# Kernel optimization log

Hardware: AMD Instinct MI355X
Metric: run time of the kernel (lower is better)

Reference implementation:

```python
import jax, jax.numpy as jnp
import numpy as np

N = 50000      # nodes
E = 800000     # edges (before self-loops)
DIN = 2        # dim_input
DEMB = 128     # dim_embedding
H = 8          # n_heads
DV = 16        # dim_values (H*DV == DEMB)
DH = 512       # dim_hidden
L = 2          # n_att_layers
K = 10         # APPNP steps
ALPHA = 0.1
EPS = 1e-5     # BatchNorm eps
NEG_SLOPE = 0.2  # GAT leaky_relu slope


def setup_inputs() -> dict:
    key = jax.random.key(0)
    ks = jax.random.split(key, 16)
    s = 0.05
    inp = {}
    inp["x"] = jax.random.normal(ks[0], (N, DIN), jnp.float32)
    inp["J"] = jax.random.uniform(ks[1], (N, 1), jnp.float32)
    inp["edge_index"] = jax.random.randint(ks[2], (2, E), 0, N, jnp.int32)
    # Lin1: Linear(dim_input+1, dim_embedding)
    inp["lin0_w"] = jax.random.normal(ks[3], (DIN + 1, DEMB), jnp.float32) * s
    inp["lin0_b"] = jnp.zeros((DEMB,), jnp.float32)
    # Per attention layer (stacked over L):
    inp["gat_w"]   = jax.random.normal(ks[4], (L, DEMB, H * DV), jnp.float32) * s
    inp["att_src"] = jax.random.normal(ks[5], (L, H, DV), jnp.float32) * s
    inp["att_dst"] = jax.random.normal(ks[6], (L, H, DV), jnp.float32) * s
    inp["lin1_w"]  = jax.random.normal(ks[7], (L, DV, DEMB), jnp.float32) * s
    inp["bn1_g"]   = jnp.ones((L, DEMB), jnp.float32)
    inp["bn1_b"]   = jnp.zeros((L, DEMB), jnp.float32)
    inp["lin2_w"]  = jax.random.normal(ks[8], (L, DEMB, DH), jnp.float32) * s
    inp["lin2_b"]  = jnp.zeros((L, DH), jnp.float32)
    inp["lin3_w"]  = jax.random.normal(ks[9], (L, DH, DEMB), jnp.float32) * s
    inp["lin3_b"]  = jnp.zeros((L, DEMB), jnp.float32)
    inp["bn2_g"]   = jnp.ones((L, DEMB), jnp.float32)
    inp["bn2_b"]   = jnp.zeros((L, DEMB), jnp.float32)
    return inp


def _bn(z, g, b):
    # BatchNorm1d over nodes, training-mode batch statistics (biased var)
    mu = z.mean(0)
    var = jnp.mean((z - mu) ** 2, axis=0)
    return g * (z - mu) * jax.lax.rsqrt(var + EPS) + b


def reference(x, J, edge_index, lin0_w, lin0_b, gat_w, att_src, att_dst,
              lin1_w, bn1_g, bn1_b, lin2_w, lin2_b, lin3_w, lin3_b,
              bn2_g, bn2_b):
    # add self-loops (PyG GATConv and APPNP defaults)
    loop = jnp.arange(N, dtype=edge_index.dtype)
    src = jnp.concatenate([edge_index[0], loop])  # message source j
    dst = jnp.concatenate([edge_index[1], loop])  # message target i

    h = jnp.concatenate([x, J], axis=1) @ lin0_w + lin0_b  # [N, DEMB]

    for l in range(L):
        # ---- GATConv ----
        xl = (h @ gat_w[l]).reshape(N, H, DV)                # [N,H,DV]
        a_s = (xl * att_src[l]).sum(-1)                      # [N,H]
        a_d = (xl * att_dst[l]).sum(-1)                      # [N,H]
        e = jax.nn.leaky_relu(a_s[src] + a_d[dst], NEG_SLOPE)  # [E',H]
        e = e - jax.ops.segment_max(e, dst, num_segments=N)[dst]
        ee = jnp.exp(e)
        alpha = ee / jax.ops.segment_sum(ee, dst, num_segments=N)[dst]
        msg = xl[src] * alpha[:, :, None]                    # [E',H,DV]
        gat_out = jax.ops.segment_sum(msg, dst, num_segments=N)  # [N,H,DV]
        # lin1 per head then sum over heads
        hsum = jnp.einsum('nhc,cd->nd', gat_out, lin1_w[l])  # [N,DEMB]
        h1 = _bn(h + hsum, bn1_g[l], bn1_b[l])
        h2 = jax.nn.relu(h1 @ lin2_w[l] + lin2_b[l]) @ lin3_w[l] + lin3_b[l]
        h = _bn(h2 + h1, bn2_g[l], bn2_b[l])

    # ---- APPNP: K steps of (1-a)*Ahat h + a*h0, Ahat = D^-1/2 (A+I) D^-1/2 ----
    deg = jax.ops.segment_sum(jnp.ones_like(dst, jnp.float32), dst, num_segments=N)
    dinv = jax.lax.rsqrt(jnp.maximum(deg, 1.0))  # self-loops guarantee deg>=1
    norm = (dinv[src] * dinv[dst])[:, None]      # [E',1]
    h0 = h

    def step(hk, _):
        agg = jax.ops.segment_sum(norm * hk[src], dst, num_segments=N)
        return (1.0 - ALPHA) * agg + ALPHA * h0, None

    h, _ = jax.lax.scan(step, h, None, length=K)
    return jnp.concatenate([h, J], axis=1)  # [N, DEMB+1]
```

## Files before the change

kernel.cpp:

```cpp
#include <hip/hip_runtime.h>

#define NN 50000
#define NP 50048
#define NMT64 782
#define NE 800000
#define EP (NE + NN)
#define DEMB 128
#define DHID 512
#define NB_SCAN 196

typedef unsigned short ushort_t;
typedef __attribute__((ext_vector_type(8))) short short8_t;
typedef __attribute__((ext_vector_type(4))) float float4_t;

__device__ __forceinline__ float bf2f(ushort_t u) {
    return __uint_as_float(((unsigned int)u) << 16);
}
__device__ __forceinline__ ushort_t f2bf(float f) {
    unsigned int x = __float_as_uint(f);
    x += 0x7fffu + ((x >> 16) & 1u);
    return (ushort_t)(x >> 16);
}
__device__ __forceinline__ float lo16(unsigned int w) { return __uint_as_float(w << 16); }
__device__ __forceinline__ float hi16(unsigned int w) { return __uint_as_float(w & 0xffff0000u); }
__device__ __forceinline__ unsigned int pack2(float a, float b) {
    return (unsigned int)f2bf(a) | ((unsigned int)f2bf(b) << 16);
}
__device__ __forceinline__ void gl_lds16(const ushort_t* g, ushort_t* l) {
    __builtin_amdgcn_global_load_lds(
        (const __attribute__((address_space(1))) void*)g,
        (__attribute__((address_space(3))) void*)l, 16, 0, 0);
}
static inline int cdiv(int a, int b) { return (a + b - 1) / b; }

__global__ void k_detect(const unsigned int* __restrict__ Jw, int* __restrict__ flag) {
    if (threadIdx.x != 0 || blockIdx.x != 0) return;
    int votes = 0;
    for (int i = 0; i < 8; ++i) {
        unsigned int w = Jw[i];
        unsigned int ex = (w >> 23) & 0xFFu;
        if ((w >> 31) == 0u && ex >= 100u && ex <= 126u) votes++;
    }
    *flag = (votes >= 6) ? 1 : 0;
}

struct CvtArgs {
    const void* src[16];
    float* dst[16];
    int n[16];
};
__global__ void k_cvt_all(CvtArgs a, const int* __restrict__ flag) {
    int which = blockIdx.y;
    int i = blockIdx.x * 256 + threadIdx.x;
    if (i >= a.n[which]) return;
    float v;
    if (*flag) v = ((const float*)a.src[which])[i];
    else       v = bf2f(((const ushort_t*)a.src[which])[i]);
    a.dst[which][i] = v;
}

struct TrArgs {
    const float* src[6];
    ushort_t* dst[6];
    int K[6];
    int Nc[6];
};
__global__ void k_tr_all(TrArgs a) {
    int which = blockIdx.y;
    int idx = blockIdx.x * 256 + threadIdx.x;
    int K = a.K[which], Nc = a.Nc[which];
    if (idx >= K * Nc) return;
    int k = idx / Nc, n = idx - k * Nc;
    a.dst[which][n * K + k] = f2bf(a.src[which][idx]);
}

__global__ void k_deg(const int* __restrict__ ei, int* __restrict__ deg) {
    int e = blockIdx.x * 256 + threadIdx.x;
    if (e >= EP) return;
    int d = (e < NE) ? ei[NE + e] : (e - NE);
    atomicAdd(&deg[d], 1);
}

__global__ void k_part(const int* __restrict__ deg, int* __restrict__ part) {
    __shared__ int sm[256];
    int i = blockIdx.x * 256 + threadIdx.x;
    int v = (i < NN) ? deg[i] : 0;
    sm[threadIdx.x] = v;
    __syncthreads();
    for (int off = 128; off > 0; off >>= 1) {
        if (threadIdx.x < off) sm[threadIdx.x] += sm[threadIdx.x + off];
        __syncthreads();
    }
    if (threadIdx.x == 0) part[blockIdx.x] = sm[0];
}

__global__ void k_scan2(const int* __restrict__ part, int* __restrict__ poff,
                        int* __restrict__ rowp) {
    __shared__ int sm[256];
    int t = threadIdx.x;
    int v = (t < NB_SCAN) ? part[t] : 0;
    sm[t] = v;
    __syncthreads();
    int incl = v;
    for (int off = 1; off < 256; off <<= 1) {
        int u = (t >= off) ? sm[t - off] : 0;
        __syncthreads();
        incl += u;
        sm[t] = incl;
        __syncthreads();
    }
    if (t < NB_SCAN) poff[t] = incl - v;
    if (t == 255) rowp[NN] = sm[255];
}

__global__ void k_rowp(const int* __restrict__ deg, const int* __restrict__ poff,
                       int* __restrict__ rowp, float* __restrict__ dinv,
                       int* __restrict__ fill) {
    __shared__ int sm[256];
    int i = blockIdx.x * 256 + threadIdx.x;
    int t = threadIdx.x;
    int v = (i < NN) ? deg[i] : 0;
    sm[t] = v;
    __syncthreads();
    int incl = v;
    for (int off = 1; off < 256; off <<= 1) {
        int u = (t >= off) ? sm[t - off] : 0;
        __syncthreads();
        incl += u;
        sm[t] = incl;
        __syncthreads();
    }
    if (i < NN) {
        int rp = poff[blockIdx.x] + incl - v;
        rowp[i] = rp;
        fill[i] = rp;
        dinv[i] = rsqrtf(fmaxf((float)v, 1.0f));
    }
}

__global__ void k_fill(const int* __restrict__ ei, int* __restrict__ fillpos,
                       ushort_t* __restrict__ col) {
    int e = blockIdx.x * 256 + threadIdx.x;
    if (e >= EP) return;
    int s, d;
    if (e < NE) { s = ei[e]; d = ei[NE + e]; } else { s = d = e - NE; }
    int pos = atomicAdd(&fillpos[d], 1);
    col[pos] = (ushort_t)s;
}

__global__ void k_lin0(const float* __restrict__ x, const float* __restrict__ J,
                       const float* __restrict__ w, const float* __restrict__ b,
                       ushort_t* __restrict__ hB) {
    int idx = blockIdx.x * 256 + threadIdx.x;
    if (idx >= NN * DEMB) return;
    int n = idx >> 7, d = idx & 127;
    float v = x[n * 2] * w[d] + x[n * 2 + 1] * w[DEMB + d] + J[n] * w[2 * DEMB + d] + b[d];
    hB[idx] = f2bf(v);
}

__global__ void k_att(const unsigned int* __restrict__ xlB, const float* __restrict__ asrc,
                      const float* __restrict__ adst, float* __restrict__ a_s,
                      float* __restrict__ a_d) {
    int idx = blockIdx.x * 256 + threadIdx.x;
    if (idx >= NN * 8) return;
    int n = idx >> 3, hh = idx & 7;
    const unsigned int* row = xlB + (size_t)n * 64 + hh * 8;
    float s = 0.f, d = 0.f;
#pragma unroll
    for (int c = 0; c < 8; ++c) {
        unsigned int w = row[c];
        float v0 = lo16(w), v1 = hi16(w);
        s += v0 * asrc[hh * 16 + 2 * c] + v1 * asrc[hh * 16 + 2 * c + 1];
        d += v0 * adst[hh * 16 + 2 * c] + v1 * adst[hh * 16 + 2 * c + 1];
    }
    a_s[idx] = s;
    a_d[idx] = d;
}

__global__ __launch_bounds__(256) void k_z1s(const ushort_t* __restrict__ hB,
                                             const float* __restrict__ g,
                                             const float* __restrict__ w1,
                                             float* __restrict__ stats) {
    int d = threadIdx.x & 127;
    int rstart = blockIdx.x * 2 + (threadIdx.x >> 7);
    int stride = gridDim.x * 2;
    float s1 = 0.f, s2 = 0.f;
    for (int r = rstart; r < NN; r += stride) {
        const float* gr = g + r * 16;
        float s = bf2f(hB[(size_t)r * DEMB + d]);
#pragma unroll
        for (int c = 0; c < 16; ++c) s += gr[c] * w1[c * DEMB + d];
        s1 += s;
        s2 += s * s;
    }
    __shared__ float b1[256], b2[256];
    b1[threadIdx.x] = s1;
    b2[threadIdx.x] = s2;
    __syncthreads();
    if (threadIdx.x < 128) {
        atomicAdd(&stats[threadIdx.x], b1[threadIdx.x] + b1[threadIdx.x + 128]);
        atomicAdd(&stats[128 + threadIdx.x], b2[threadIdx.x] + b2[threadIdx.x + 128]);
    }
}

__global__ void k_bnapply1(const ushort_t* __restrict__ hB, const float* __restrict__ g,
                           const float* __restrict__ w1, const float* __restrict__ stats,
                           const float* __restrict__ gam, const float* __restrict__ bet,
                           ushort_t* __restrict__ outB) {
    int idx = blockIdx.x * 256 + threadIdx.x;
    if (idx >= NN * DEMB) return;
    int n = idx >> 7, d = idx & 127;
    float s = bf2f(hB[idx]);
    const float* gr = g + n * 16;
#pragma unroll
    for (int c = 0; c < 16; ++c) s += gr[c] * w1[c * DEMB + d];
    const float invN = 1.0f / (float)NN;
    float mu = stats[d] * invN;
    float var = stats[128 + d] * invN - mu * mu;
    float rs = rsqrtf(fmaxf(var, 0.f) + 1e-5f);
    float v = gam[d] * (s - mu) * rs + bet[d];
    outB[idx] = f2bf(v);
}

__global__ void k_bnapply(const ushort_t* __restrict__ zB, const float* __restrict__ stats,
                          const float* __restrict__ gam, const float* __restrict__ bet,
                          ushort_t* __restrict__ outB) {
    int idx = blockIdx.x * 256 + threadIdx.x;
    if (idx >= NN * DEMB) return;
    int d = idx & 127;
    const float invN = 1.0f / (float)NN;
    float mu = stats[d] * invN;
    float var = stats[128 + d] * invN - mu * mu;
    float rs = rsqrtf(fmaxf(var, 0.f) + 1e-5f);
    float v = gam[d] * (bf2f(zB[idx]) - mu) * rs + bet[d];
    outB[idx] = f2bf(v);
}

__global__ void k_bnapply_fin(const unsigned int* __restrict__ zB, const float* __restrict__ stats,
                              const float* __restrict__ gam, const float* __restrict__ bet,
                              const float* __restrict__ dinv,
                              unsigned int* __restrict__ hs, unsigned int* __restrict__ h0p) {
    int idx = blockIdx.x * 256 + threadIdx.x;
    if (idx >= NN * 64) return;
    int n = idx >> 6, d0 = (idx & 63) * 2;
    const float invN = 1.0f / (float)NN;
    unsigned int zw = zB[idx];
    float z0 = lo16(zw), z1 = hi16(zw);
    float mu0 = stats[d0] * invN, mu1 = stats[d0 + 1] * invN;
    float v0 = stats[128 + d0] * invN - mu0 * mu0;
    float v1 = stats[128 + d0 + 1] * invN - mu1 * mu1;
    float rs0 = rsqrtf(fmaxf(v0, 0.f) + 1e-5f);
    float rs1 = rsqrtf(fmaxf(v1, 0.f) + 1e-5f);
    float a = gam[d0] * (z0 - mu0) * rs0 + bet[d0];
    float b = gam[d0 + 1] * (z1 - mu1) * rs1 + bet[d0 + 1];
    float di = dinv[n];
    hs[idx] = pack2(di * a, di * b);
    h0p[idx] = pack2(a, b);
}

__global__ __launch_bounds__(256) void k_gat(const int* __restrict__ rowp,
                                             const ushort_t* __restrict__ col,
                                             const float* __restrict__ a_s, const float* __restrict__ a_d,
                                             const unsigned int* __restrict__ xlB, float* __restrict__ g) {
    int wid = (blockIdx.x * 256 + threadIdx.x) >> 6;
    int lane = threadIdx.x & 63;
    if (wid >= NN) return;
    int p0 = rowp[wid], p1 = rowp[wid + 1];
    int hh = lane >> 3;
    float ad2 = a_d[wid * 8 + hh];
    float acc0 = 0.f, acc1 = 0.f, s = 0.f;
    int p = p0;
    while (p < p1) {
        int cnt = p1 - p;
        if (cnt > 64) cnt = 64;
        int pl = p + lane;
        int jv = (int)col[pl < p1 ? pl : (p1 - 1)];
        int i = 0;
        for (; i + 8 <= cnt; i += 8) {
            int j0 = __shfl(jv, i),     j1 = __shfl(jv, i + 1);
            int j2 = __shfl(jv, i + 2), j3 = __shfl(jv, i + 3);
            int j4 = __shfl(jv, i + 4), j5 = __shfl(jv, i + 5);
            int j6 = __shfl(jv, i + 6), j7 = __shfl(jv, i + 7);
            float e0 = a_s[j0 * 8 + hh] + ad2, e1 = a_s[j1 * 8 + hh] + ad2;
            float e2 = a_s[j2 * 8 + hh] + ad2, e3 = a_s[j3 * 8 + hh] + ad2;
            float e4 = a_s[j4 * 8 + hh] + ad2, e5 = a_s[j5 * 8 + hh] + ad2;
            float e6 = a_s[j6 * 8 + hh] + ad2, e7 = a_s[j7 * 8 + hh] + ad2;
            unsigned int w0 = xlB[j0 * 64 + lane], w1 = xlB[j1 * 64 + lane];
            unsigned int w2 = xlB[j2 * 64 + lane], w3 = xlB[j3 * 64 + lane];
            unsigned int w4 = xlB[j4 * 64 + lane], w5 = xlB[j5 * 64 + lane];
            unsigned int w6 = xlB[j6 * 64 + lane], w7 = xlB[j7 * 64 + lane];
            e0 = e0 > 0.f ? e0 : 0.2f * e0;  e1 = e1 > 0.f ? e1 : 0.2f * e1;
            e2 = e2 > 0.f ? e2 : 0.2f * e2;  e3 = e3 > 0.f ? e3 : 0.2f * e3;
            e4 = e4 > 0.f ? e4 : 0.2f * e4;  e5 = e5 > 0.f ? e5 : 0.2f * e5;
            e6 = e6 > 0.f ? e6 : 0.2f * e6;  e7 = e7 > 0.f ? e7 : 0.2f * e7;
            float al0 = __expf(e0), al1 = __expf(e1), al2 = __expf(e2), al3 = __expf(e3);
            float al4 = __expf(e4), al5 = __expf(e5), al6 = __expf(e6), al7 = __expf(e7);
            s += al0 + al1 + al2 + al3 + al4 + al5 + al6 + al7;
            acc0 += al0 * lo16(w0) + al1 * lo16(w1) + al2 * lo16(w2) + al3 * lo16(w3) +
                    al4 * lo16(w4) + al5 * lo16(w5) + al6 * lo16(w6) + al7 * lo16(w7);
            acc1 += al0 * hi16(w0) + al1 * hi16(w1) + al2 * hi16(w2) + al3 * hi16(w3) +
                    al4 * hi16(w4) + al5 * hi16(w5) + al6 * hi16(w6) + al7 * hi16(w7);
        }
        for (; i < cnt; ++i) {
            int j = __shfl(jv, i);
            float e = a_s[j * 8 + hh] + ad2;
            e = e > 0.f ? e : 0.2f * e;
            float al = __expf(e);
            unsigned int w = xlB[j * 64 + lane];
            s += al;
            acc0 += al * lo16(w);
            acc1 += al * hi16(w);
        }
        p += cnt;
    }
    float inv = 1.f / s;
    acc0 *= inv;
    acc1 *= inv;
    acc0 += __shfl_xor(acc0, 8);  acc1 += __shfl_xor(acc1, 8);
    acc0 += __shfl_xor(acc0, 16); acc1 += __shfl_xor(acc1, 16);
    acc0 += __shfl_xor(acc0, 32); acc1 += __shfl_xor(acc1, 32);
    if (lane < 8) ((float2*)g)[wid * 8 + lane] = make_float2(acc0, acc1);
}

__global__ __launch_bounds__(256) void k_appnp(const int* __restrict__ rowp,
                                               const ushort_t* __restrict__ col,
                                               const float* __restrict__ dinv,
                                               const unsigned int* __restrict__ hs,
                                               const unsigned int* __restrict__ h0p,
                                               unsigned int* __restrict__ hs_out,
                                               const float* __restrict__ Jf,
                                               const int* __restrict__ flag,
                                               void* __restrict__ out, int writeOut) {
    int wid = (blockIdx.x * 256 + threadIdx.x) >> 6;
    int lane = threadIdx.x & 63;
    if (wid >= NN) return;
    int p0 = rowp[wid], p1 = rowp[wid + 1];
    float di = dinv[wid];
    unsigned int hw = h0p[(size_t)wid * 64 + lane];
    float a0 = 0.f, a1 = 0.f;
    int p = p0;
    while (p < p1) {
        int cnt = p1 - p;
        if (cnt > 64) cnt = 64;
        int pl = p + lane;
        int jv = (int)col[pl < p1 ? pl : (p1 - 1)];
        int i = 0;
        for (; i + 8 <= cnt; i += 8) {
            int j0 = __shfl(jv, i),     j1 = __shfl(jv, i + 1);
            int j2 = __shfl(jv, i + 2), j3 = __shfl(jv, i + 3);
            int j4 = __shfl(jv, i + 4), j5 = __shfl(jv, i + 5);
            int j6 = __shfl(jv, i + 6), j7 = __shfl(jv, i + 7);
            unsigned int w0 = hs[j0 * 64 + lane], w1 = hs[j1 * 64 + lane];
            unsigned int w2 = hs[j2 * 64 + lane], w3 = hs[j3 * 64 + lane];
            unsigned int w4 = hs[j4 * 64 + lane], w5 = hs[j5 * 64 + lane];
            unsigned int w6 = hs[j6 * 64 + lane], w7 = hs[j7 * 64 + lane];
            a0 += lo16(w0) + lo16(w1) + lo16(w2) + lo16(w3) +
                  lo16(w4) + lo16(w5) + lo16(w6) + lo16(w7);
            a1 += hi16(w0) + hi16(w1) + hi16(w2) + hi16(w3) +
                  hi16(w4) + hi16(w5) + hi16(w6) + hi16(w7);
        }
        for (; i < cnt; ++i) {
            int j = __shfl(jv, i);
            unsigned int w = hs[j * 64 + lane];
            a0 += lo16(w);
            a1 += hi16(w);
        }
        p += cnt;
    }
    float n0 = 0.9f * di * a0 + 0.1f * lo16(hw);
    float n1 = 0.9f * di * a1 + 0.1f * hi16(hw);
    if (!writeOut) {
        hs_out[(size_t)wid * 64 + lane] = pack2(di * n0, di * n1);
    } else {
        size_t base = (size_t)wid * 129;
        if (*flag) {
            float* o = (float*)out;
            o[base + 2 * lane] = n0;
            o[base + 2 * lane + 1] = n1;
            if (lane == 0) o[base + 128] = Jf[wid];
        } else {
            ushort_t* o = (ushort_t*)out;
            o[base + 2 * lane] = f2bf(n0);
            o[base + 2 * lane + 1] = f2bf(n1);
            if (lane == 0) o[base + 128] = f2bf(Jf[wid]);
        }
    }
}

template <int MODE>
__global__ __launch_bounds__(256) void k_gemm64(const ushort_t* __restrict__ A,
                                                const ushort_t* __restrict__ Bt,
                                                int M, int K, int Nc,
                                                const float* __restrict__ bias,
                                                const ushort_t* __restrict__ res,
                                                ushort_t* __restrict__ outB,
                                                float* __restrict__ stats) {
    __shared__ __align__(16) ushort_t lsA[2][64 * 32];
    __shared__ __align__(16) ushort_t lsB[2][128 * 32];
    int t = threadIdx.x;
    int m0 = blockIdx.x * 64;
    int n0 = blockIdx.y * 128;
    int w = t >> 6, lane = t & 63;
    int row16 = lane & 15, quad = lane >> 4;
    int nbase = w * 32;
    float4_t acc[8];
#pragma unroll
    for (int i = 0; i < 8; ++i) acc[i] = (float4_t){0.f, 0.f, 0.f, 0.f};
    int lrow = lane >> 2;
    int lcol = (lane & 3) * 8;
    const ushort_t* gA  = A  + (size_t)(m0 + w * 16 + lrow) * K + lcol;
    const ushort_t* gB0 = Bt + (size_t)(n0 + w * 32 + lrow) * K + lcol;
    const ushort_t* gB1 = Bt + (size_t)(n0 + w * 32 + 16 + lrow) * K + lcol;
    ushort_t* dA  = &lsA[0][0] + (w * 16) * 32;
    ushort_t* dB0 = &lsB[0][0] + (w * 32) * 32;
    ushort_t* dB1 = &lsB[0][0] + (w * 32 + 16) * 32;
    const int bufStrideA = 64 * 32, bufStrideB = 128 * 32;
    const int nK = K >> 5;
    gl_lds16(gA, dA);
    gl_lds16(gB0, dB0);
    gl_lds16(gB1, dB1);
    for (int kb = 0; kb < nK; ++kb) {
        __syncthreads();
        int nb = kb + 1;
        if (nb < nK) {
            int b = nb & 1;
            int k0 = nb << 5;
            gl_lds16(gA + k0, dA + b * bufStrideA);
            gl_lds16(gB0 + k0, dB0 + b * bufStrideB);
            gl_lds16(gB1 + k0, dB1 + b * bufStrideB);
        }
        const ushort_t* la = &lsA[kb & 1][0];
        const ushort_t* lb = &lsB[kb & 1][0];
        short8_t afr[4], bfr[2];
#pragma unroll
        for (int i = 0; i < 4; ++i)
            afr[i] = *(const short8_t*)(la + (i * 16 + row16) * 32 + quad * 8);
#pragma unroll
        for (int i = 0; i < 2; ++i)
            bfr[i] = *(const short8_t*)(lb + (nbase + i * 16 + row16) * 32 + quad * 8);
#pragma unroll
        for (int mt = 0; mt < 4; ++mt)
#pragma unroll
            for (int nt = 0; nt < 2; ++nt)
                acc[mt * 2 + nt] = __builtin_amdgcn_mfma_f32_16x16x32_bf16(
                    afr[mt], bfr[nt], acc[mt * 2 + nt], 0, 0, 0);
    }
#pragma unroll
    for (int mt = 0; mt < 4; ++mt) {
#pragma unroll
        for (int nt = 0; nt < 2; ++nt) {
            int cc = n0 + nbase + nt * 16 + row16;
#pragma unroll
            for (int r = 0; r < 4; ++r) {
                int rr = m0 + mt * 16 + quad * 4 + r;
                if (rr < M) {
                    outB[(size_t)rr * Nc + cc] = f2bf(acc[mt * 2 + nt][r]);
                }
            }
        }
    }
}

__global__ __launch_bounds__(256, 2) void k_ffn(const ushort_t* __restrict__ A,
                                                const ushort_t* __restrict__ W2t,
                                                const ushort_t* __restrict__ W3t,
                                                const float* __restrict__ b2,
                                                const float* __restrict__ b3,
                                                const ushort_t* __restrict__ res,
                                                ushort_t* __restrict__ outB,
                                                float* __restrict__ stats) {
    __shared__ __align__(16) ushort_t lsA[4 * 64 * 32];
    __shared__ __align__(16) ushort_t lsW2[4 * 64 * 32];
    __shared__ __align__(16) ushort_t lsW3[2][2 * 128 * 32];
    __shared__ __align__(16) ushort_t lsH[4][2 * 16 * 32];
    __shared__ float s1[128], s2[128];
    int t = threadIdx.x;
    int w = t >> 6, lane = t & 63;
    int m0 = blockIdx.x * 64;
    int row16 = lane & 15, quad = lane >> 4;
    int sw = (row16 >> 2) & 3;
    int srow = lane >> 2;
    int klin = lane & 3;

    if (t < 128) { s1[t] = 0.f; s2[t] = 0.f; }

#pragma unroll
    for (int i = 0; i < 4; ++i) {
        int row = i * 16 + srow;
        int kc = klin ^ ((row >> 2) & 3);
        gl_lds16(A + (size_t)(m0 + row) * 128 + w * 32 + kc * 8,
                 lsA + w * 2048 + i * 512);
    }
#pragma unroll
    for (int i = 0; i < 4; ++i) {
        int n = i * 16 + srow;
        int kc = klin ^ ((n >> 2) & 3);
        gl_lds16(W2t + (size_t)n * 128 + w * 32 + kc * 8,
                 lsW2 + w * 2048 + i * 512);
    }
#pragma unroll
    for (int i = 0; i < 4; ++i) {
        int f = w * 4 + i;
        int ks = f >> 3;
        int n = (f & 7) * 16 + srow;
        int kc = klin ^ ((n >> 2) & 3);
        gl_lds16(W3t + (size_t)n * 512 + ks * 32 + kc * 8,
                 &lsW3[0][0] + f * 512);
    }
    __syncthreads();

    short8_t afrA[4];
#pragma unroll
    for (int kb = 0; kb < 4; ++kb)
        afrA[kb] = *(const short8_t*)(lsA + kb * 2048 + (w * 16 + row16) * 32 + (quad ^ sw) * 8);

    float4_t accz[8];
#pragma unroll
    for (int i = 0; i < 8; ++i) accz[i] = (float4_t){0.f, 0.f, 0.f, 0.f};

    for (int c = 0; c < 8; ++c) {
        float b2v[4];
#pragma unroll
        for (int nt = 0; nt < 4; ++nt) b2v[nt] = b2[c * 64 + nt * 16 + row16];
        float4_t acch[4];
#pragma unroll
        for (int i = 0; i < 4; ++i) acch[i] = (float4_t){0.f, 0.f, 0.f, 0.f};
#pragma unroll
        for (int kb = 0; kb < 4; ++kb) {
            short8_t bfr[4];
#pragma unroll
            for (int nt = 0; nt < 4; ++nt) {
                int n = nt * 16 + row16;
                bfr[nt] = *(const short8_t*)(lsW2 + kb * 2048 + n * 32 + (quad ^ sw) * 8);
            }
#pragma unroll
            for (int nt = 0; nt < 4; ++nt)
                acch[nt] = __builtin_amdgcn_mfma_f32_16x16x32_bf16(afrA[kb], bfr[nt],
                                                                   acch[nt], 0, 0, 0);
        }
#pragma unroll
        for (int nt = 0; nt < 4; ++nt) {
            int ks = nt >> 1;
#pragma unroll
            for (int r = 0; r < 4; ++r) {
                int row = quad * 4 + r;
                int colk = (nt & 1) * 16 + row16;
                int scol = (colk & 7) | ((((colk >> 3) ^ quad)) << 3);
                float v = acch[nt][r] + b2v[nt];
                v = v > 0.f ? v : 0.f;
                lsH[w][ks * 512 + row * 32 + scol] = f2bf(v);
            }
        }
        __syncthreads();

        if (c + 1 < 8) {
#pragma unroll
            for (int i = 0; i < 4; ++i) {
                int n = i * 16 + srow;
                int kc = klin ^ ((n >> 2) & 3);
                gl_lds16(W2t + (size_t)((c + 1) * 64 + n) * 128 + w * 32 + kc * 8,
                         lsW2 + w * 2048 + i * 512);
            }
            ushort_t* w3dst = &lsW3[(c + 1) & 1][0];
#pragma unroll
            for (int i = 0; i < 4; ++i) {
                int f = w * 4 + i;
                int ks = f >> 3;
                int n = (f & 7) * 16 + srow;
                int kc = klin ^ ((n >> 2) & 3);
                gl_lds16(W3t + (size_t)n * 512 + (c + 1) * 64 + ks * 32 + kc * 8,
                         w3dst + f * 512);
            }
        }
        const ushort_t* w3src = &lsW3[c & 1][0];
#pragma unroll
        for (int ks = 0; ks < 2; ++ks) {
            short8_t afrH = *(const short8_t*)(&lsH[w][0] + ks * 512 + row16 * 32 +
                                               (quad ^ sw) * 8);
            short8_t bfr[8];
#pragma unroll
            for (int nt = 0; nt < 8; ++nt) {
                int n = nt * 16 + row16;
                bfr[nt] = *(const short8_t*)(w3src + ks * 4096 + n * 32 + (quad ^ sw) * 8);
            }
#pragma unroll
            for (int nt = 0; nt < 8; ++nt)
                accz[nt] = __builtin_amdgcn_mfma_f32_16x16x32_bf16(afrH, bfr[nt],
                                                                   accz[nt], 0, 0, 0);
        }
        __syncthreads();
    }

#pragma unroll
    for (int nt = 0; nt < 8; ++nt) {
        int cc = nt * 16 + row16;
        float bv = b3[cc];
        float ls = 0.f, lq = 0.f;
#pragma unroll
        for (int r = 0; r < 4; ++r) {
            int rr = m0 + w * 16 + quad * 4 + r;
            if (rr < NN) {
                float v = accz[nt][r] + bv + bf2f(res[(size_t)rr * 128 + cc]);
                outB[(size_t)rr * 128 + cc] = f2bf(v);
                ls += v;
                lq += v * v;
            }
        }
        atomicAdd(&s1[cc], ls);
        atomicAdd(&s2[cc], lq);
    }
    __syncthreads();
    if (t < 128) {
        atomicAdd(&stats[t], s1[t]);
        atomicAdd(&stats[128 + t], s2[t]);
    }
}

extern "C" void kernel_launch(void* const* d_in, const int* in_sizes, int n_in,
                              void* d_out, int out_size, void* d_ws, size_t ws_size,
                              hipStream_t stream) {
    const int* ei = (const int*)d_in[2];

    char* p = (char*)d_ws;
    auto alloc = [&](size_t bytes) {
        void* r = (void*)p;
        p += (bytes + 255) & ~(size_t)255;
        return r;
    };
    ushort_t* hB    = (ushort_t*)alloc((size_t)NP * DEMB * 2);
    ushort_t* h1B   = (ushort_t*)alloc((size_t)NP * DEMB * 2);
    ushort_t* xlB   = (ushort_t*)alloc((size_t)NN * DEMB * 2);
    unsigned int* hsA  = (unsigned int*)alloc((size_t)NN * 64 * 4);
    unsigned int* hsB_ = (unsigned int*)alloc((size_t)NN * 64 * 4);
    unsigned int* h0p  = (unsigned int*)alloc((size_t)NN * 64 * 4);
    float*    asv   = (float*)alloc((size_t)NN * 8 * 4);
    float*    adv   = (float*)alloc((size_t)NN * 8 * 4);
    float*    gv    = (float*)alloc((size_t)NN * 16 * 4);
    float*    dinvv = (float*)alloc((size_t)NN * 4);
    float*    stats = (float*)alloc(4 * 256 * 4);
    int*      deg   = (int*)alloc((size_t)NN * 4);
    int*      rowp  = (int*)alloc((size_t)(NN + 1) * 4);
    int*      fill  = (int*)alloc((size_t)NN * 4);
    ushort_t* colv  = (ushort_t*)alloc((size_t)EP * 2);
    int*      part  = (int*)alloc(NB_SCAN * 4);
    int*      poff  = (int*)alloc(NB_SCAN * 4);
    int*      flag  = (int*)alloc(256);
    ushort_t* wtg   = (ushort_t*)alloc((size_t)2 * 128 * 128 * 2);
    ushort_t* wt2   = (ushort_t*)alloc((size_t)2 * 512 * 128 * 2);
    ushort_t* wt3   = (ushort_t*)alloc((size_t)2 * 128 * 512 * 2);
    float* xf   = (float*)alloc((size_t)NN * 2 * 4);
    float* Jf   = (float*)alloc((size_t)NN * 4);
    float* l0wF = (float*)alloc(384 * 4);
    float* l0bF = (float*)alloc(128 * 4);
    float* gwF  = (float*)alloc(32768 * 4);
    float* asF  = (float*)alloc(256 * 4);
    float* adF  = (float*)alloc(256 * 4);
    float* w1F  = (float*)alloc(4096 * 4);
    float* b1gF = (float*)alloc(256 * 4);
    float* b1bF = (float*)alloc(256 * 4);
    float* w2F  = (float*)alloc(131072 * 4);
    float* b2F  = (float*)alloc(1024 * 4);
    float* w3F  = (float*)alloc(131072 * 4);
    float* b3F  = (float*)alloc(256 * 4);
    float* b2gF = (float*)alloc(256 * 4);
    float* b2bF = (float*)alloc(256 * 4);

    k_detect<<<1, 64, 0, stream>>>((const unsigned int*)d_in[1], flag);
    CvtArgs ca;
    {
        const int srcIdx[16] = {0, 1, 3, 4, 5, 6, 7, 8, 9, 10, 11, 12, 13, 14, 15, 16};
        float* dsts[16] = {xf, Jf, l0wF, l0bF, gwF, asF, adF, w1F, b1gF, b1bF,
                           w2F, b2F, w3F, b3F, b2gF, b2bF};
        const int ns[16] = {NN * 2, NN, 384, 128, 32768, 256, 256, 4096, 256, 256,
                            131072, 1024, 131072, 256, 256, 256};
        for (int i = 0; i < 16; ++i) { ca.src[i] = d_in[srcIdx[i]]; ca.dst[i] = dsts[i]; ca.n[i] = ns[i]; }
    }
    k_cvt_all<<<dim3(cdiv(131072, 256), 16), 256, 0, stream>>>(ca, flag);

    hipMemsetAsync(deg, 0, (size_t)NN * 4, stream);
    hipMemsetAsync(stats, 0, 4 * 256 * 4, stream);
    k_deg<<<cdiv(EP, 256), 256, 0, stream>>>(ei, deg);
    k_part<<<NB_SCAN, 256, 0, stream>>>(deg, part);
    k_scan2<<<1, 256, 0, stream>>>(part, poff, rowp);
    k_rowp<<<NB_SCAN, 256, 0, stream>>>(deg, poff, rowp, dinvv, fill);
    k_fill<<<cdiv(EP, 256), 256, 0, stream>>>(ei, fill, colv);

    TrArgs ta;
    {
        const float* srcs[6] = {gwF, gwF + 16384, w2F, w2F + 65536, w3F, w3F + 65536};
        ushort_t* dsts[6] = {wtg, wtg + 16384, wt2, wt2 + 65536, wt3, wt3 + 65536};
        const int Ks[6] = {128, 128, 128, 128, 512, 512};
        const int Ncs[6] = {128, 128, 512, 512, 128, 128};
        for (int i = 0; i < 6; ++i) { ta.src[i] = srcs[i]; ta.dst[i] = dsts[i]; ta.K[i] = Ks[i]; ta.Nc[i] = Ncs[i]; }
    }
    k_tr_all<<<dim3(cdiv(65536, 256), 6), 256, 0, stream>>>(ta);

    k_lin0<<<cdiv(NN * DEMB, 256), 256, 0, stream>>>(xf, Jf, l0wF, l0bF, hB);

    for (int l = 0; l < 2; ++l) {
        float* st1 = stats + (l * 2 + 0) * 256;
        float* st2 = stats + (l * 2 + 1) * 256;
        ushort_t* zB = xlB;
        k_gemm64<3><<<dim3(NMT64, 1), 256, 0, stream>>>(hB, wtg + l * 16384, NN, 128, 128,
                                                        nullptr, nullptr, xlB, nullptr);
        k_att<<<cdiv(NN * 8, 256), 256, 0, stream>>>((const unsigned int*)xlB, asF + l * 128,
                                                     adF + l * 128, asv, adv);
        k_gat<<<cdiv(NN * 64, 256), 256, 0, stream>>>(rowp, colv, asv, adv,
                                                      (const unsigned int*)xlB, gv);
        k_z1s<<<512, 256, 0, stream>>>(hB, gv, w1F + l * 2048, st1);
        k_bnapply1<<<cdiv(NN * DEMB, 256), 256, 0, stream>>>(hB, gv, w1F + l * 2048, st1,
                                                             b1gF + l * 128, b1bF + l * 128,
                                                             h1B);
        k_ffn<<<NMT64, 256, 0, stream>>>(h1B, wt2 + l * 65536, wt3 + l * 65536,
                                         b2F + l * 512, b3F + l * 128, h1B, zB, st2);
        if (l == 0) {
            k_bnapply<<<cdiv(NN * DEMB, 256), 256, 0, stream>>>(zB, st2, b2gF, b2bF, hB);
        } else {
            k_bnapply_fin<<<cdiv(NN * 64, 256), 256, 0, stream>>>((const unsigned int*)zB, st2,
                                                                  b2gF + 128, b2bF + 128,
                                                                  dinvv, hsA, h0p);
        }
    }

    unsigned int* pin = hsA;
    unsigned int* pout = hsB_;
    for (int k = 0; k < 10; ++k) {
        int last = (k == 9) ? 1 : 0;
        k_appnp<<<cdiv(NN * 64, 256), 256, 0, stream>>>(rowp, colv, dinvv, pin, h0p, pout,
                                                        Jf, flag, d_out, last);
        unsigned int* tmp = pout;
        pout = pin;
        pin = tmp;
    }
}
```

Baseline: 902.1 us.

## Double-buffer W2 in FFN kernel, drop per-chunk barrier, permute W3 K-order

The fused FFN kernel now double-buffers the W2 tile and issues the next chunk's W2/W3 loads before the current chunk's GEMM1, removing one barrier per chunk. The hidden tile is written as packed bf16 pairs using an XOR-swizzled layout. The W3 transpose permutes its K index so those packed writes line up with the MFMA fragment order. LDS is reused by aliasing the A staging buffer for the hidden tile and the BN stats, which depends on an added sync and on the permutation matching the packing exactly.

```diff
diff --git a/kernel.cpp b/kernel.cpp
--- a/kernel.cpp
+++ b/kernel.cpp
@@ -64,6 +64,7 @@
     ushort_t* dst[6];
     int K[6];
     int Nc[6];
+    int perm[6];
 };
 __global__ void k_tr_all(TrArgs a) {
     int which = blockIdx.y;
@@ -71,7 +72,14 @@
     int K = a.K[which], Nc = a.Nc[which];
     if (idx >= K * Nc) return;
     int k = idx / Nc, n = idx - k * Nc;
-    a.dst[which][n * K + k] = f2bf(a.src[which][idx]);
+    int kd = k;
+    if (a.perm[which]) {
+        int kk = k & 63;
+        int ks = kk >> 5, k5 = kk & 31;
+        int u = (k5 >> 4) & 1, q = (k5 >> 2) & 3, tt = k5 & 3;
+        kd = (k & ~63) | (ks * 32 + q * 8 + tt * 2 + u);
+    }
+    a.dst[which][n * K + kd] = f2bf(a.src[which][idx]);
 }
 
 __global__ void k_deg(const int* __restrict__ ei, int* __restrict__ deg) {
@@ -469,11 +477,9 @@
                                                 const ushort_t* __restrict__ res,
                                                 ushort_t* __restrict__ outB,
                                                 float* __restrict__ stats) {
-    __shared__ __align__(16) ushort_t lsA[4 * 64 * 32];
-    __shared__ __align__(16) ushort_t lsW2[4 * 64 * 32];
-    __shared__ __align__(16) ushort_t lsW3[2][2 * 128 * 32];
-    __shared__ __align__(16) ushort_t lsH[4][2 * 16 * 32];
-    __shared__ float s1[128], s2[128];
+    __shared__ __align__(16) ushort_t sW2[2][4 * 64 * 32];
+    __shared__ __align__(16) ushort_t sW3[2][2 * 128 * 32];
+    __shared__ __align__(16) ushort_t sAH[4][2048];
     int t = threadIdx.x;
     int w = t >> 6, lane = t & 63;
     int m0 = blockIdx.x * 64;
@@ -482,21 +488,19 @@
     int srow = lane >> 2;
     int klin = lane & 3;
 
-    if (t < 128) { s1[t] = 0.f; s2[t] = 0.f; }
-
 #pragma unroll
     for (int i = 0; i < 4; ++i) {
         int row = i * 16 + srow;
         int kc = klin ^ ((row >> 2) & 3);
         gl_lds16(A + (size_t)(m0 + row) * 128 + w * 32 + kc * 8,
-                 lsA + w * 2048 + i * 512);
+                 &sAH[0][0] + w * 2048 + i * 512);
     }
 #pragma unroll
     for (int i = 0; i < 4; ++i) {
         int n = i * 16 + srow;
         int kc = klin ^ ((n >> 2) & 3);
         gl_lds16(W2t + (size_t)n * 128 + w * 32 + kc * 8,
-                 lsW2 + w * 2048 + i * 512);
+                 &sW2[0][0] + w * 2048 + i * 512);
     }
 #pragma unroll
     for (int i = 0; i < 4; ++i) {
@@ -505,63 +509,36 @@
         int n = (f & 7) * 16 + srow;
         int kc = klin ^ ((n >> 2) & 3);
         gl_lds16(W3t + (size_t)n * 512 + ks * 32 + kc * 8,
-                 &lsW3[0][0] + f * 512);
+                 &sW3[0][0] + f * 512);
     }
     __syncthreads();
 
     short8_t afrA[4];
 #pragma unroll
     for (int kb = 0; kb < 4; ++kb)
-        afrA[kb] = *(const short8_t*)(lsA + kb * 2048 + (w * 16 + row16) * 32 + (quad ^ sw) * 8);
+        afrA[kb] = *(const short8_t*)(&sAH[0][0] + kb * 2048 + (w * 16 + row16) * 32 + (quad ^ sw) * 8);
+    __syncthreads();
+
+    float* s1 = (float*)&sAH[0][1024];
+    float* s2 = s1 + 128;
+    if (t < 128) { s1[t] = 0.f; s2[t] = 0.f; }
+    ushort_t* Hbase = &sAH[w][0];
 
     float4_t accz[8];
 #pragma unroll
     for (int i = 0; i < 8; ++i) accz[i] = (float4_t){0.f, 0.f, 0.f, 0.f};
 
     for (int c = 0; c < 8; ++c) {
-        float b2v[4];
-#pragma unroll
-        for (int nt = 0; nt < 4; ++nt) b2v[nt] = b2[c * 64 + nt * 16 + row16];
-        float4_t acch[4];
-#pragma unroll
-        for (int i = 0; i < 4; ++i) acch[i] = (float4_t){0.f, 0.f, 0.f, 0.f};
-#pragma unroll
-        for (int kb = 0; kb < 4; ++kb) {
-            short8_t bfr[4];
-#pragma unroll
-            for (int nt = 0; nt < 4; ++nt) {
-                int n = nt * 16 + row16;
-                bfr[nt] = *(const short8_t*)(lsW2 + kb * 2048 + n * 32 + (quad ^ sw) * 8);
-            }
-#pragma unroll
-            for (int nt = 0; nt < 4; ++nt)
-                acch[nt] = __builtin_amdgcn_mfma_f32_16x16x32_bf16(afrA[kb], bfr[nt],
-                                                                   acch[nt], 0, 0, 0);
-        }
-#pragma unroll
-        for (int nt = 0; nt < 4; ++nt) {
-            int ks = nt >> 1;
-#pragma unroll
-            for (int r = 0; r < 4; ++r) {
-                int row = quad * 4 + r;
-                int colk = (nt & 1) * 16 + row16;
-                int scol = (colk & 7) | ((((colk >> 3) ^ quad)) << 3);
-                float v = acch[nt][r] + b2v[nt];
-                v = v > 0.f ? v : 0.f;
-                lsH[w][ks * 512 + row * 32 + scol] = f2bf(v);
-            }
-        }
-        __syncthreads();
-
-        if (c + 1 < 8) {
+        int cb = c & 1;
+        if (c < 7) {
+            int nb = cb ^ 1;
 #pragma unroll
             for (int i = 0; i < 4; ++i) {
                 int n = i * 16 + srow;
                 int kc = klin ^ ((n >> 2) & 3);
                 gl_lds16(W2t + (size_t)((c + 1) * 64 + n) * 128 + w * 32 + kc * 8,
-                         lsW2 + w * 2048 + i * 512);
+                         &sW2[nb][0] + w * 2048 + i * 512);
             }
-            ushort_t* w3dst = &lsW3[(c + 1) & 1][0];
 #pragma unroll
             for (int i = 0; i < 4; ++i) {
                 int f = w * 4 + i;
@@ -569,20 +546,47 @@
                 int n = (f & 7) * 16 + srow;
                 int kc = klin ^ ((n >> 2) & 3);
                 gl_lds16(W3t + (size_t)n * 512 + (c + 1) * 64 + ks * 32 + kc * 8,
-                         w3dst + f * 512);
+                         &sW3[nb][0] + f * 512);
             }
         }
-        const ushort_t* w3src = &lsW3[c & 1][0];
+        float4_t acch[4];
+#pragma unroll
+        for (int i = 0; i < 4; ++i) acch[i] = (float4_t){0.f, 0.f, 0.f, 0.f};
+#pragma unroll
+        for (int kb = 0; kb < 4; ++kb) {
+            short8_t bfr[4];
+#pragma unroll
+            for (int nt = 0; nt < 4; ++nt)
+                bfr[nt] = *(const short8_t*)(&sW2[cb][0] + kb * 2048 + (nt * 16 + row16) * 32 + (quad ^ sw) * 8);
+#pragma unroll
+            for (int nt = 0; nt < 4; ++nt)
+                acch[nt] = __builtin_amdgcn_mfma_f32_16x16x32_bf16(afrA[kb], bfr[nt],
+                                                                   acch[nt], 0, 0, 0);
+        }
+        {
+            float b2v[4];
+#pragma unroll
+            for (int nt = 0; nt < 4; ++nt) b2v[nt] = b2[c * 64 + nt * 16 + row16];
+#pragma unroll
+            for (int r = 0; r < 4; ++r) {
+                int row = quad * 4 + r;
+                float v0 = acch[0][r] + b2v[0]; v0 = v0 > 0.f ? v0 : 0.f;
+                float v1 = acch[1][r] + b2v[1]; v1 = v1 > 0.f ? v1 : 0.f;
+                float v2 = acch[2][r] + b2v[2]; v2 = v2 > 0.f ? v2 : 0.f;
+                float v3 = acch[3][r] + b2v[3]; v3 = v3 > 0.f ? v3 : 0.f;
+                int byteA = row * 128 + ((((row16 >> 2) ^ (row & 7))) << 4) + (row16 & 3) * 4;
+                *(unsigned int*)((char*)Hbase + byteA) = pack2(v0, v1);
+                *(unsigned int*)((char*)Hbase + (byteA ^ 64)) = pack2(v2, v3);
+            }
+        }
 #pragma unroll
         for (int ks = 0; ks < 2; ++ks) {
-            short8_t afrH = *(const short8_t*)(&lsH[w][0] + ks * 512 + row16 * 32 +
-                                               (quad ^ sw) * 8);
+            short8_t afrH = *(const short8_t*)((char*)Hbase + row16 * 128 +
+                                               ((((ks << 2) | quad) ^ (row16 & 7)) << 4));
             short8_t bfr[8];
 #pragma unroll
-            for (int nt = 0; nt < 8; ++nt) {
-                int n = nt * 16 + row16;
-                bfr[nt] = *(const short8_t*)(w3src + ks * 4096 + n * 32 + (quad ^ sw) * 8);
-            }
+            for (int nt = 0; nt < 8; ++nt)
+                bfr[nt] = *(const short8_t*)(&sW3[cb][0] + ks * 4096 + (nt * 16 + row16) * 32 + (quad ^ sw) * 8);
 #pragma unroll
             for (int nt = 0; nt < 8; ++nt)
                 accz[nt] = __builtin_amdgcn_mfma_f32_16x16x32_bf16(afrH, bfr[nt],
@@ -691,7 +695,11 @@
         ushort_t* dsts[6] = {wtg, wtg + 16384, wt2, wt2 + 65536, wt3, wt3 + 65536};
         const int Ks[6] = {128, 128, 128, 128, 512, 512};
         const int Ncs[6] = {128, 128, 512, 512, 128, 128};
-        for (int i = 0; i < 6; ++i) { ta.src[i] = srcs[i]; ta.dst[i] = dsts[i]; ta.K[i] = Ks[i]; ta.Nc[i] = Ncs[i]; }
+        const int perms[6] = {0, 0, 0, 0, 1, 1};
+        for (int i = 0; i < 6; ++i) {
+            ta.src[i] = srcs[i]; ta.dst[i] = dsts[i]; ta.K[i] = Ks[i]; ta.Nc[i] = Ncs[i];
+            ta.perm[i] = perms[i];
+        }
     }
     k_tr_all<<<dim3(cdiv(65536, 256), 6), 256, 0, stream>>>(ta);
 
```

After: 903.4 us. About the same (+0.1%).
